# Kernel tuning notes

Measured on AMD Instinct MI355X. Metric: run time of the kernel, lower is better.

The kernel has to match this reference:

```python
import jax, jax.numpy as jnp
import numpy as np

# SymBranch: delta_i = |h_i - h_pi(i)| (0 if unpaired) -> ResNetMLP -> per-graph
# mean pairwise-L2 scores -> softmax(s/tau) -> weighted sum pooling.
# ResNetMLP (reconstructed, eval mode: dropout=identity):
#   h = x @ W_in + b_in
#   for each block: h = h + relu(LN(h @ Wk + bk))
#   z = LN_out(h @ W_out + b_out)   (last_norm=True)

B, NPG, IN_DIM, HID, EMB, NBLK = 64, 1024, 64, 256, 128, 3
TAU = 0.25
LN_EPS = 1e-5


def _ln(x, g, b):
    mu = jnp.mean(x, axis=-1, keepdims=True)
    var = jnp.var(x, axis=-1, keepdims=True)
    return (x - mu) * jax.lax.rsqrt(var + LN_EPS) * g + b


def setup_inputs() -> dict:
    key = jax.random.key(0)
    ks = jax.random.split(key, 8)
    N = B * NPG
    H = jax.random.normal(ks[0], (N, IN_DIM), jnp.float32)
    batch_ptr = jnp.arange(B + 1, dtype=jnp.int32) * NPG  # equal-size graphs
    # symmetric pairs: node i in first half of each graph paired with i + NPG/2
    half = NPG // 2
    base = (jnp.arange(B, dtype=jnp.int32) * NPG)[:, None]
    li = (base + jnp.arange(half, dtype=jnp.int32)[None, :]).reshape(-1)
    ri = (base + half + jnp.arange(half, dtype=jnp.int32)[None, :]).reshape(-1)
    pairs = jnp.stack([li, ri], axis=1)  # [M,2] global indices
    W_in = jax.random.normal(ks[1], (IN_DIM, HID), jnp.float32) * (1.0 / np.sqrt(IN_DIM))
    b_in = jnp.zeros((HID,), jnp.float32)
    Wb = jax.random.normal(ks[2], (NBLK, HID, HID), jnp.float32) * (1.0 / np.sqrt(HID))
    bb = jnp.zeros((NBLK, HID), jnp.float32)
    lng = jnp.ones((NBLK, HID), jnp.float32)
    lnb = jnp.zeros((NBLK, HID), jnp.float32)
    W_out = jax.random.normal(ks[3], (HID, EMB), jnp.float32) * (1.0 / np.sqrt(HID))
    b_out = jnp.zeros((EMB,), jnp.float32)
    lnf_g = jnp.ones((EMB,), jnp.float32)
    lnf_b = jnp.zeros((EMB,), jnp.float32)
    return dict(H=H, batch_ptr=batch_ptr, pairs=pairs, W_in=W_in, b_in=b_in,
                Wb=Wb, bb=bb, lng=lng, lnb=lnb, W_out=W_out, b_out=b_out,
                lnf_g=lnf_g, lnf_b=lnf_b)


def reference(H, batch_ptr, pairs, W_in, b_in, Wb, bb, lng, lnb, W_out, b_out, lnf_g, lnf_b):
    # gather-diff-scatter: delta_i = |h_i - h_pair(i)|, 0 for unpaired nodes
    li, ri = pairs[:, 0], pairs[:, 1]
    diff = jnp.abs(H[li] - H[ri])                       # [M, in_dim]
    delta = jnp.zeros_like(H).at[li].set(diff).at[ri].set(diff)  # [N, in_dim]
    # ResNetMLP (eval: dropout off)
    h = delta @ W_in + b_in                             # [N, HID]
    for k in range(NBLK):
        h = h + jax.nn.relu(_ln(h @ Wb[k] + bb[k], lng[k], lnb[k]))
    z = _ln(h @ W_out + b_out, lnf_g, lnf_b)            # [N, EMB]
    # per-graph mean pairwise L2 (graphs are equal-sized: reshape is the batched
    # equivalent of the python loop over batch_ptr slices)
    zb = z.reshape(B, NPG, EMB)
    sq = jnp.sum(zb * zb, axis=-1)                      # [B, n]
    d2 = sq[:, :, None] + sq[:, None, :] - 2.0 * jnp.einsum('bne,bme->bnm', zb, zb)
    dist = jnp.sqrt(jnp.clip(d2, 1e-12))                # [B, n, n]
    s = jnp.mean(dist, axis=-1)                         # [B, n]
    w = jax.nn.softmax(s / TAU, axis=-1)                # [B, n]
    f = jnp.einsum('bn,bne->be', w, zb)                 # [B, EMB]
    return f, w
```

## Files before the change

kernel.cpp:

```cpp
#include <hip/hip_runtime.h>
#include <hip/hip_bf16.h>

using bf16 = __hip_bfloat16;
typedef __attribute__((ext_vector_type(8))) short  bfrag;
typedef __attribute__((ext_vector_type(4))) float  ffrag;

#define DEVFN static __device__ __forceinline__

constexpr int BATCH  = 64;
constexpr int NPG    = 1024;
constexpr int IN_DIM = 64;
constexpr int HID    = 256;
constexpr int EMB    = 128;
constexpr int NPAIR  = BATCH * NPG / 2;
constexpr float TAU    = 0.25f;
constexpr float LN_EPS = 1e-5f;

constexpr int MT  = 32;
constexpr int LDH = 264;

DEVFN float b2f(unsigned short u) {
    union { unsigned int i; float f; } x; x.i = ((unsigned int)u) << 16; return x.f;
}
DEVFN unsigned short f2b(float f) {
    bf16 h = __float2bfloat16(f);
    unsigned short u; __builtin_memcpy(&u, &h, 2); return u;
}

__global__ __launch_bounds__(256) void prep_w_kernel(
    const float* __restrict__ Win, const float* __restrict__ Wb,
    const float* __restrict__ Wout,
    unsigned short* __restrict__ WinT, unsigned short* __restrict__ WbT,
    unsigned short* __restrict__ WoutT)
{
    __shared__ short t[64][72];
    const int bid = blockIdx.x, tid = threadIdx.x;
    const float* S; unsigned short* D; int N_, K_, k0, n0;
    if (bid < 48) {
        int mat = bid >> 4, tt = bid & 15;
        S = Wb + mat * 65536; D = WbT + mat * 65536;
        K_ = 256; N_ = 256; k0 = (tt >> 2) * 64; n0 = (tt & 3) * 64;
    } else if (bid < 52) {
        int tt = bid - 48;
        S = Win; D = WinT; K_ = 64; N_ = 256; k0 = 0; n0 = tt * 64;
    } else {
        int tt = bid - 52;
        S = Wout; D = WoutT; K_ = 256; N_ = 128; k0 = (tt >> 1) * 64; n0 = (tt & 1) * 64;
    }
    #pragma unroll
    for (int it = 0; it < 4; ++it) {
        int idx = it * 256 + tid;
        int kk = idx >> 4, n4 = idx & 15;
        float4 v = *(const float4*)(S + (size_t)(k0 + kk) * N_ + n0 + n4 * 4);
        t[n4 * 4 + 0][kk] = (short)f2b(v.x);
        t[n4 * 4 + 1][kk] = (short)f2b(v.y);
        t[n4 * 4 + 2][kk] = (short)f2b(v.z);
        t[n4 * 4 + 3][kk] = (short)f2b(v.w);
    }
    __syncthreads();
    const int KB = K_ >> 5, nb = n0 >> 6;
    #pragma unroll
    for (int it = 0; it < 2; ++it) {
        int u = it * 256 + tid;
        int kbL = u >> 8, rem = u & 255;
        int j = rem >> 6, ln = rem & 63;
        int l16 = ln & 15, qd = ln >> 4;
        bfrag val = *(const bfrag*)&t[j * 16 + l16][kbL * 32 + qd * 8];
        size_t dst = (((size_t)(nb * KB + (k0 >> 5) + kbL) * 4 + j) * 64 + ln) * 8;
        *(bfrag*)(D + dst) = val;
    }
}

template<int K, int N, int MODE>
DEVFN void gemm_phase(short* hbuf, float (*part)[8],
                      const unsigned short* __restrict__ Bf,
                      const float* __restrict__ bias,
                      const float* __restrict__ gamma,
                      const float* __restrict__ beta,
                      unsigned short* __restrict__ Zb,
                      float* __restrict__ sqout, int m0)
{
    constexpr int WN = N / 64;
    constexpr int WM = 4 / WN;
    constexpr int RM = (MT / WM) / 16;
    constexpr int RN = 4;
    constexpr int KB = K / 32;

    const int tid  = threadIdx.x;
    const int wave = tid >> 6, lane = tid & 63;
    const int quad = lane >> 4, l16 = lane & 15;
    const int wrow = (wave / WN) * (MT / WM);
    const int wcol = (wave % WN) * 64;

    __syncthreads();

    ffrag acc[RM][RN];
    #pragma unroll
    for (int i = 0; i < RM; i++)
        #pragma unroll
        for (int j = 0; j < RN; j++)
            #pragma unroll
            for (int r = 0; r < 4; r++) acc[i][j][r] = 0.f;

    const unsigned short* bq = Bf + (size_t)(wcol >> 6) * KB * 2048
                                  + (size_t)lane * 8;

    bfrag Ball[KB][RN];
    #pragma unroll
    for (int kb = 0; kb < KB; kb++)
        #pragma unroll
        for (int j = 0; j < RN; j++)
            Ball[kb][j] = *(const bfrag*)(bq + ((size_t)kb * 4 + j) * 512);

    bfrag Ab[2][RM];
    #pragma unroll
    for (int i = 0; i < RM; i++)
        Ab[0][i] = *(const bfrag*)&hbuf[(wrow + i * 16 + l16) * LDH + quad * 8];

    __builtin_amdgcn_sched_barrier(0);

    #pragma unroll
    for (int kb = 0; kb < KB; kb++) {
        const int cur = kb & 1, nxt = cur ^ 1;
        if (kb + 1 < KB) {
            #pragma unroll
            for (int i = 0; i < RM; i++)
                Ab[nxt][i] = *(const bfrag*)&hbuf[(wrow + i * 16 + l16) * LDH
                                                  + (kb + 1) * 32 + quad * 8];
        }
        #pragma unroll
        for (int i = 0; i < RM; i++)
            #pragma unroll
            for (int j = 0; j < RN; j++)
                acc[i][j] = __builtin_amdgcn_mfma_f32_16x16x32_bf16(
                                Ab[cur][i], Ball[kb][j], acc[i][j], 0, 0, 0);
    }

    float bia[RN], gam[RN], bet[RN];
    #pragma unroll
    for (int j = 0; j < RN; j++) {
        int gcol = wcol + j * 16 + l16;
        bia[j] = bias[gcol];
        if constexpr (MODE != 0) { gam[j] = gamma[gcol]; bet[j] = beta[gcol]; }
    }
    #pragma unroll
    for (int i = 0; i < RM; i++)
        #pragma unroll
        for (int j = 0; j < RN; j++)
            #pragma unroll
            for (int r = 0; r < 4; r++) acc[i][j][r] += bia[j];

    if constexpr (MODE == 0) {
        __syncthreads();
        #pragma unroll
        for (int i = 0; i < RM; i++)
            #pragma unroll
            for (int j = 0; j < RN; j++) {
                int gcol = wcol + j * 16 + l16;
                #pragma unroll
                for (int r = 0; r < 4; r++) {
                    int row = wrow + i * 16 + quad * 4 + r;
                    hbuf[row * LDH + gcol] = (short)f2b(acc[i][j][r]);
                }
            }
    } else {
        #pragma unroll
        for (int i = 0; i < RM; i++) {
            #pragma unroll
            for (int r = 0; r < 4; r++) {
                float s1 = 0.f, s2 = 0.f;
                #pragma unroll
                for (int j = 0; j < RN; j++) {
                    float x = acc[i][j][r]; s1 += x; s2 += x * x;
                }
                #pragma unroll
                for (int m = 1; m < 16; m <<= 1) {
                    s1 += __shfl_xor(s1, m); s2 += __shfl_xor(s2, m);
                }
                if (l16 == 0) {
                    int row = wrow + i * 16 + quad * 4 + r;
                    part[row][(wave % WN) * 2]     = s1;
                    part[row][(wave % WN) * 2 + 1] = s2;
                }
            }
        }
        __syncthreads();
        float s3a[RM][4];
        #pragma unroll
        for (int i = 0; i < RM; i++) {
            #pragma unroll
            for (int r = 0; r < 4; r++) {
                int row = wrow + i * 16 + quad * 4 + r;
                float s1 = 0.f, s2 = 0.f;
                #pragma unroll
                for (int wn = 0; wn < WN; wn++) {
                    s1 += part[row][wn * 2]; s2 += part[row][wn * 2 + 1];
                }
                float mean = s1 * (1.f / N);
                float rstd = rsqrtf(s2 * (1.f / N) - mean * mean + LN_EPS);
                float s3 = 0.f;
                #pragma unroll
                for (int j = 0; j < RN; j++) {
                    int gcol = wcol + j * 16 + l16;
                    float y = (acc[i][j][r] - mean) * rstd * gam[j] + bet[j];
                    if constexpr (MODE == 1) {
                        float res = b2f((unsigned short)hbuf[row * LDH + gcol]);
                        y = fmaxf(y, 0.f) + res;
                        hbuf[row * LDH + gcol] = (short)f2b(y);
                    } else {
                        unsigned short ub = f2b(y);
                        Zb[(size_t)(m0 + row) * EMB + gcol] = ub;
                        float yr = b2f(ub);
                        s3 += yr * yr;
                    }
                }
                s3a[i][r] = s3;
            }
        }
        if constexpr (MODE == 2) {
            __syncthreads();
            #pragma unroll
            for (int i = 0; i < RM; i++)
                #pragma unroll
                for (int r = 0; r < 4; r++) {
                    float s3 = s3a[i][r];
                    #pragma unroll
                    for (int m = 1; m < 16; m <<= 1) s3 += __shfl_xor(s3, m);
                    if (l16 == 0) {
                        int row = wrow + i * 16 + quad * 4 + r;
                        part[row][wave % WN] = s3;
                    }
                }
            __syncthreads();
            if (l16 == 0 && (wave % WN) == 0) {
                #pragma unroll
                for (int i = 0; i < RM; i++)
                    #pragma unroll
                    for (int r = 0; r < 4; r++) {
                        int row = wrow + i * 16 + quad * 4 + r;
                        float t = 0.f;
                        #pragma unroll
                        for (int wn = 0; wn < WN; wn++) t += part[row][wn];
                        sqout[m0 + row] = t;
                    }
            }
        }
    }
}

__global__ __launch_bounds__(256, 2) void fused_mlp_kernel(
    const float* __restrict__ H, const int* __restrict__ pairs,
    const unsigned short* __restrict__ WinT,
    const unsigned short* __restrict__ WbT,
    const unsigned short* __restrict__ WoutT,
    const float* __restrict__ b_in,  const float* __restrict__ bb,
    const float* __restrict__ lng,   const float* __restrict__ lnb,
    const float* __restrict__ b_out, const float* __restrict__ lnf_g,
    const float* __restrict__ lnf_b,
    unsigned short* __restrict__ Zb, float* __restrict__ sq)
{
    __shared__ __align__(16) short hbuf[MT * LDH];
    __shared__ float part[MT][8];

    const int tid = threadIdx.x;
    const int m0  = blockIdx.x * MT;

    #pragma unroll
    for (int it = 0; it < 2; ++it) {
        int idx = tid + it * 256;
        int r = idx >> 4, c4 = idx & 15;
        int p = m0 + r;
        int li = pairs[2 * p], ri = pairs[2 * p + 1];
        float4 a = *(const float4*)(H + (size_t)li * IN_DIM + c4 * 4);
        float4 b = *(const float4*)(H + (size_t)ri * IN_DIM + c4 * 4);
        short4 s;
        s.x = (short)f2b(fabsf(a.x - b.x));
        s.y = (short)f2b(fabsf(a.y - b.y));
        s.z = (short)f2b(fabsf(a.z - b.z));
        s.w = (short)f2b(fabsf(a.w - b.w));
        *(short4*)&hbuf[r * LDH + c4 * 4] = s;
    }

    gemm_phase<IN_DIM, HID, 0>(hbuf, part, WinT, b_in,
                               nullptr, nullptr, nullptr, nullptr, m0);
    gemm_phase<HID, HID, 1>(hbuf, part, WbT,
                            bb,       lng,       lnb,       nullptr, nullptr, m0);
    gemm_phase<HID, HID, 1>(hbuf, part, WbT + 65536,
                            bb + 256, lng + 256, lnb + 256, nullptr, nullptr, m0);
    gemm_phase<HID, HID, 1>(hbuf, part, WbT + 131072,
                            bb + 512, lng + 512, lnb + 512, nullptr, nullptr, m0);
    gemm_phase<HID, EMB, 2>(hbuf, part, WoutT, b_out,
                            lnf_g, lnf_b, Zb, sq, m0);
}

__global__ __launch_bounds__(256) void gram_kernel(
    const unsigned short* __restrict__ Z, const float* __restrict__ sq,
    float* __restrict__ srowP)
{
    constexpr int LDU = EMB + 8;
    __shared__ __align__(16) short Brows[2][64 * LDU];

    const int batch = blockIdx.x >> 4;
    const int rt    = (blockIdx.x >> 1) & 7;
    const int hf    = blockIdx.x & 1;
    const int tid = threadIdx.x, wave = tid >> 6, lane = tid & 63;
    const int quad = lane >> 4, l16 = lane & 15;
    const int urow0 = batch * 512;
    const int ar0   = urow0 + rt * 64;
    const int arow  = ar0 + wave * 16 + l16;

    bfrag a4[4];
    #pragma unroll
    for (int kk = 0; kk < 4; kk++)
        a4[kk] = *(const bfrag*)(Z + (size_t)arow * EMB + kk * 32 + quad * 8);

    float rs[4] = {0.f, 0.f, 0.f, 0.f};
    float sqr[4];
    #pragma unroll
    for (int r = 0; r < 4; r++)
        sqr[r] = sq[ar0 + wave * 16 + quad * 4 + r];

    const int sr = tid >> 4, sc = (tid & 15) * 8;
    bfrag g[4];
    #pragma unroll
    for (int it = 0; it < 4; ++it)
        g[it] = *(const bfrag*)(Z + (size_t)(urow0 + hf * 256 + it * 16 + sr) * EMB + sc);

    for (int c = 0; c < 4; ++c) {
        const int cur = c & 1;
        #pragma unroll
        for (int it = 0; it < 4; ++it)
            *(bfrag*)&Brows[cur][(it * 16 + sr) * LDU + sc] = g[it];
        if (c < 3) {
            #pragma unroll
            for (int it = 0; it < 4; ++it)
                g[it] = *(const bfrag*)(Z + (size_t)(urow0 + hf * 256 + (c + 1) * 64
                                                     + it * 16 + sr) * EMB + sc);
        }
        __syncthreads();
        int ch = hf * 4 + c;
        ffrag acc[4];
        #pragma unroll
        for (int j = 0; j < 4; j++)
            #pragma unroll
            for (int r = 0; r < 4; r++) acc[j][r] = 0.f;
        #pragma unroll
        for (int kk = 0; kk < 4; ++kk)
            #pragma unroll
            for (int j = 0; j < 4; j++) {
                bfrag b = *(const bfrag*)&Brows[cur][(j * 16 + l16) * LDU
                                                     + kk * 32 + quad * 8];
                acc[j] = __builtin_amdgcn_mfma_f32_16x16x32_bf16(a4[kk], b,
                                                                 acc[j], 0, 0, 0);
            }
        #pragma unroll
        for (int j = 0; j < 4; j++) {
            float sqc = sq[urow0 + ch * 64 + j * 16 + l16];
            #pragma unroll
            for (int r = 0; r < 4; r++) {
                float d2 = sqr[r] + sqc - 2.f * acc[j][r];
                rs[r] += sqrtf(fmaxf(d2, 1e-12f));
            }
        }
    }
    #pragma unroll
    for (int r = 0; r < 4; r++) {
        float v = rs[r];
        v += __shfl_xor(v, 1); v += __shfl_xor(v, 2);
        v += __shfl_xor(v, 4); v += __shfl_xor(v, 8);
        if (l16 == 0)
            srowP[hf * (BATCH * 512) + batch * 512 + rt * 64
                  + wave * 16 + quad * 4 + r] = v;
    }
}

__global__ __launch_bounds__(1024) void softmax_f_kernel(
    const float* __restrict__ srowP, const unsigned short* __restrict__ Z,
    float* __restrict__ fout, float* __restrict__ wout)
{
    const int b = blockIdx.x, tid = threadIdx.x;
    __shared__ float wsh[512];
    __shared__ float red[16];
    __shared__ float fred[8][128];
    constexpr float SC = (1.f / 512.f) * (1.f / TAU);

    const int wv = tid >> 6, lane = tid & 63;
    float l0 = 0.f, e0 = 0.f;
    if (tid < 512) {
        l0 = (srowP[b * 512 + tid] + srowP[BATCH * 512 + b * 512 + tid]) * SC;
        float mx = l0;
        #pragma unroll
        for (int m = 1; m < 64; m <<= 1) mx = fmaxf(mx, __shfl_xor(mx, m));
        if (lane == 0) red[wv] = mx;
    }
    __syncthreads();
    float mx = red[0];
    #pragma unroll
    for (int i = 1; i < 8; i++) mx = fmaxf(mx, red[i]);
    if (tid < 512) {
        e0 = expf(l0 - mx);
        float s = e0;
        #pragma unroll
        for (int m = 1; m < 64; m <<= 1) s += __shfl_xor(s, m);
        if (lane == 0) red[8 + wv] = s;
    }
    __syncthreads();
    float sum = 0.f;
    #pragma unroll
    for (int i = 0; i < 8; i++) sum += red[8 + i];
    float inv = 1.f / sum;
    if (tid < 512) wsh[tid] = e0 * inv;
    __syncthreads();
    wout[b * 1024 + tid] = wsh[tid & 511] * 0.5f;

    const int g = tid >> 7, e = tid & 127;
    const unsigned short* zp = Z + (size_t)(b * 512 + g * 64) * EMB + e;
    float acc = 0.f;
    #pragma unroll 8
    for (int c = 0; c < 64; c++)
        acc += wsh[g * 64 + c] * b2f(zp[(size_t)c * EMB]);
    fred[g][e] = acc;
    __syncthreads();
    if (tid < 128) {
        float t = 0.f;
        #pragma unroll
        for (int gg = 0; gg < 8; gg++) t += fred[gg][e];
        fout[b * EMB + e] = t;
    }
}

extern "C" void kernel_launch(void* const* d_in, const int* in_sizes, int n_in,
                              void* d_out, int out_size, void* d_ws, size_t ws_size,
                              hipStream_t stream)
{
    (void)in_sizes; (void)n_in; (void)out_size; (void)ws_size;
    const float* H     = (const float*)d_in[0];
    const int*   pairs = (const int*)d_in[2];
    const float* W_in  = (const float*)d_in[3];
    const float* b_in  = (const float*)d_in[4];
    const float* Wb    = (const float*)d_in[5];
    const float* bb    = (const float*)d_in[6];
    const float* lng   = (const float*)d_in[7];
    const float* lnb   = (const float*)d_in[8];
    const float* W_out = (const float*)d_in[9];
    const float* b_out = (const float*)d_in[10];
    const float* lnf_g = (const float*)d_in[11];
    const float* lnf_b = (const float*)d_in[12];

    float* f_out = (float*)d_out;
    float* w_out = (float*)d_out + BATCH * EMB;

    char* ws = (char*)d_ws;
    size_t off = 0;
    auto carve = [&](size_t bytes) -> void* {
        void* p = ws + off;
        off += (bytes + 255) & ~(size_t)255;
        return p;
    };
    unsigned short* WinT  = (unsigned short*)carve((size_t)HID * IN_DIM * 2);
    unsigned short* WbT   = (unsigned short*)carve((size_t)3 * HID * HID * 2);
    unsigned short* WoutT = (unsigned short*)carve((size_t)EMB * HID * 2);
    unsigned short* Zb    = (unsigned short*)carve((size_t)NPAIR * EMB * 2);
    float*          sq    = (float*)carve((size_t)NPAIR * 4);
    float*          srowP = (float*)carve((size_t)2 * BATCH * 512 * 4);

    prep_w_kernel<<<60, 256, 0, stream>>>(W_in, Wb, W_out, WinT, WbT, WoutT);

    fused_mlp_kernel<<<NPAIR / MT, 256, 0, stream>>>(
        H, pairs, WinT, WbT, WoutT,
        b_in, bb, lng, lnb, b_out, lnf_g, lnf_b, Zb, sq);

    gram_kernel<<<BATCH * 16, 256, 0, stream>>>(Zb, sq, srowP);
    softmax_f_kernel<<<BATCH, 1024, 0, stream>>>(srowP, Zb, f_out, w_out);
}
```

Before: 152.5 us.

## Stream MLP weight fragments via global_load_lds double buffer to cut registers

Result: slower. 162.3 us (+6.5%).

```diff
diff --git a/kernel.cpp b/kernel.cpp
--- a/kernel.cpp
+++ b/kernel.cpp
@@ -25,6 +25,12 @@
 DEVFN unsigned short f2b(float f) {
     bf16 h = __float2bfloat16(f);
     unsigned short u; __builtin_memcpy(&u, &h, 2); return u;
+}
+
+DEVFN void dma16(const unsigned short* g, short* l) {
+    typedef __attribute__((address_space(3))) unsigned int  lds_u32;
+    typedef __attribute__((address_space(1))) const unsigned int glb_u32;
+    __builtin_amdgcn_global_load_lds((glb_u32*)g, (lds_u32*)l, 16, 0, 0);
 }
 
 __global__ __launch_bounds__(256) void prep_w_kernel(
@@ -73,6 +79,7 @@
 
 template<int K, int N, int MODE>
 DEVFN void gemm_phase(short* hbuf, float (*part)[8],
+                      short (*Bsh)[2][4][512],
                       const unsigned short* __restrict__ Bf,
                       const float* __restrict__ bias,
                       const float* __restrict__ gamma,
@@ -105,35 +112,40 @@
     const unsigned short* bq = Bf + (size_t)(wcol >> 6) * KB * 2048
                                   + (size_t)lane * 8;
 
-    bfrag Ball[KB][RN];
-    #pragma unroll
-    for (int kb = 0; kb < KB; kb++)
-        #pragma unroll
-        for (int j = 0; j < RN; j++)
-            Ball[kb][j] = *(const bfrag*)(bq + ((size_t)kb * 4 + j) * 512);
+    #pragma unroll
+    for (int j = 0; j < RN; j++)
+        dma16(bq + j * 512, &Bsh[wave][0][j][0]);
 
     bfrag Ab[2][RM];
     #pragma unroll
     for (int i = 0; i < RM; i++)
         Ab[0][i] = *(const bfrag*)&hbuf[(wrow + i * 16 + l16) * LDH + quad * 8];
 
-    __builtin_amdgcn_sched_barrier(0);
-
     #pragma unroll
     for (int kb = 0; kb < KB; kb++) {
-        const int cur = kb & 1, nxt = cur ^ 1;
+        const int cur = kb & 1;
+        asm volatile("s_waitcnt vmcnt(0)" ::: "memory");
+        bfrag Bv[RN];
+        #pragma unroll
+        for (int j = 0; j < RN; j++)
+            Bv[j] = *(const bfrag*)((const short*)&Bsh[wave][cur][j][0] + lane * 8);
         if (kb + 1 < KB) {
             #pragma unroll
             for (int i = 0; i < RM; i++)
-                Ab[nxt][i] = *(const bfrag*)&hbuf[(wrow + i * 16 + l16) * LDH
-                                                  + (kb + 1) * 32 + quad * 8];
+                Ab[cur ^ 1][i] = *(const bfrag*)&hbuf[(wrow + i * 16 + l16) * LDH
+                                                      + (kb + 1) * 32 + quad * 8];
+            asm volatile("" ::: "memory");
+            #pragma unroll
+            for (int j = 0; j < RN; j++)
+                dma16(bq + ((size_t)(kb + 1) * 4 + j) * 512,
+                      &Bsh[wave][cur ^ 1][j][0]);
         }
         #pragma unroll
         for (int i = 0; i < RM; i++)
             #pragma unroll
             for (int j = 0; j < RN; j++)
                 acc[i][j] = __builtin_amdgcn_mfma_f32_16x16x32_bf16(
-                                Ab[cur][i], Ball[kb][j], acc[i][j], 0, 0, 0);
+                                Ab[cur][i], Bv[j], acc[i][j], 0, 0, 0);
     }
 
     float bia[RN], gam[RN], bet[RN];
@@ -248,7 +260,7 @@
     }
 }
 
-__global__ __launch_bounds__(256, 2) void fused_mlp_kernel(
+__global__ __launch_bounds__(256, 3) void fused_mlp_kernel(
     const float* __restrict__ H, const int* __restrict__ pairs,
     const unsigned short* __restrict__ WinT,
     const unsigned short* __restrict__ WbT,
@@ -260,6 +272,7 @@
     unsigned short* __restrict__ Zb, float* __restrict__ sq)
 {
     __shared__ __align__(16) short hbuf[MT * LDH];
+    __shared__ __align__(16) short Bsh[4][2][4][512];
     __shared__ float part[MT][8];
 
     const int tid = threadIdx.x;
@@ -281,15 +294,15 @@
         *(short4*)&hbuf[r * LDH + c4 * 4] = s;
     }
 
-    gemm_phase<IN_DIM, HID, 0>(hbuf, part, WinT, b_in,
+    gemm_phase<IN_DIM, HID, 0>(hbuf, part, Bsh, WinT, b_in,
                                nullptr, nullptr, nullptr, nullptr, m0);
-    gemm_phase<HID, HID, 1>(hbuf, part, WbT,
+    gemm_phase<HID, HID, 1>(hbuf, part, Bsh, WbT,
                             bb,       lng,       lnb,       nullptr, nullptr, m0);
-    gemm_phase<HID, HID, 1>(hbuf, part, WbT + 65536,
+    gemm_phase<HID, HID, 1>(hbuf, part, Bsh, WbT + 65536,
                             bb + 256, lng + 256, lnb + 256, nullptr, nullptr, m0);
-    gemm_phase<HID, HID, 1>(hbuf, part, WbT + 131072,
+    gemm_phase<HID, HID, 1>(hbuf, part, Bsh, WbT + 131072,
                             bb + 512, lng + 512, lnb + 512, nullptr, nullptr, m0);
-    gemm_phase<HID, EMB, 2>(hbuf, part, WoutT, b_out,
+    gemm_phase<HID, EMB, 2>(hbuf, part, Bsh, WoutT, b_out,
                             lnf_g, lnf_b, Zb, sq, m0);
 }
 
```
